# Optimization experiments

Hardware: AMD Instinct MI355X
Metric: run time of the kernel (lower is better)

The kernel has to match this reference:

```python
import jax, jax.numpy as jnp
import numpy as np
import math

FS = 256
NUM_SHOT = 5


def pe_table(L, d=FS):
    pos = np.arange(L, dtype=np.float32)[:, None]
    div = np.exp(np.arange(0, d, 2, dtype=np.float32) * (-math.log(10000.0) / float(d)))
    pe = np.zeros((L, d), dtype=np.float32)
    pe[:, 0::2] = np.sin(pos * div)
    pe[:, 1::2] = np.cos(pos * div)
    return jnp.asarray(pe)


def _conv(x, w, b, stride=1):
    pad = [(1, 1), (1, 1)] if w.shape[2] == 3 else [(0, 0), (0, 0)]
    y = jax.lax.conv_general_dilated(x, w, (stride, stride), pad,
                                     dimension_numbers=('NCHW', 'OIHW', 'NCHW'))
    return y + b[None, :, None, None]


def _up2(x):
    return jnp.repeat(jnp.repeat(x, 2, axis=2), 2, axis=3)


def setup_inputs() -> dict:
    key = jax.random.key(0)
    ks = iter(jax.random.split(key, 40))
    n = lambda shape, s=0.02: jax.random.normal(next(ks), shape, dtype=jnp.float32) * s
    inp = {
        'C3': jax.random.normal(next(ks), (8, 512, 40, 40), dtype=jnp.float32),
        'C4': jax.random.normal(next(ks), (8, 1024, 20, 20), dtype=jnp.float32),
        'C5': jax.random.normal(next(ks), (8, 2048, 10, 10), dtype=jnp.float32),
        'S3': jax.random.normal(next(ks), (40, 512, 40, 40), dtype=jnp.float32),
        'S4': jax.random.normal(next(ks), (40, 1024, 20, 20), dtype=jnp.float32),
        'S5': jax.random.normal(next(ks), (40, 2048, 10, 10), dtype=jnp.float32),
        'w_p3_1': n((FS, 512, 1, 1)), 'b_p3_1': jnp.zeros((FS,), jnp.float32),
        'w_p3_2': n((FS, FS, 3, 3)), 'b_p3_2': jnp.zeros((FS,), jnp.float32),
        'w_p4_1': n((FS, 1024, 1, 1)), 'b_p4_1': jnp.zeros((FS,), jnp.float32),
        'w_p4_2': n((FS, FS, 3, 3)), 'b_p4_2': jnp.zeros((FS,), jnp.float32),
        'w_p5_1': n((FS, 2048, 1, 1)), 'b_p5_1': jnp.zeros((FS,), jnp.float32),
        'w_p5_2': n((FS, FS, 3, 3)), 'b_p5_2': jnp.zeros((FS,), jnp.float32),
        'w_p6': n((FS, 2048, 3, 3)), 'b_p6': jnp.zeros((FS,), jnp.float32),
        'w_p7': n((FS, FS, 3, 3)), 'b_p7': jnp.zeros((FS,), jnp.float32),
        'wq': n((FS, FS), 0.01), 'bq': jnp.zeros((FS,), jnp.float32),
        'wk': n((FS, FS), 0.01), 'bk': jnp.zeros((FS,), jnp.float32),
    }
    return inp


def reference(C3, C4, C5, S3, S4, S5,
              w_p3_1, b_p3_1, w_p3_2, b_p3_2,
              w_p4_1, b_p4_1, w_p4_2, b_p4_2,
              w_p5_1, b_p5_1, w_p5_2, b_p5_2,
              w_p6, b_p6, w_p7, b_p7, wq, bq, wk, bk):
    B = C3.shape[0]
    # lateral 1x1 convs (shared between query and support)
    P5x = _conv(C5, w_p5_1, b_p5_1)
    P4x = _conv(C4, w_p4_1, b_p4_1)
    P3x = _conv(C3, w_p3_1, b_p3_1)
    P5s = _conv(S5, w_p5_1, b_p5_1)
    P4s = _conv(S4, w_p4_1, b_p4_1)
    P3s = _conv(S3, w_p3_1, b_p3_1)
    # P6/P7 heads
    P6x = _conv(C5, w_p6, b_p6, stride=2)
    P7x = _conv(jax.nn.relu(P6x), w_p7, b_p7, stride=2)
    P6s = _conv(S5, w_p6, b_p6, stride=2)
    P7s = _conv(jax.nn.relu(P6s), w_p7, b_p7, stride=2)
    # query-side top-down FPN
    P4x = _up2(P5x) + P4x
    P5x2 = _conv(P5x, w_p5_2, b_p5_2)
    P3x = P3x + _up2(P4x)
    P4x2 = _conv(P4x, w_p4_2, b_p4_2)
    P3x2 = _conv(P3x, w_p3_2, b_p3_2)
    # support: [B*S, C, h, w] -> [S, B, C, h, w]
    split = lambda x: x.reshape(B, NUM_SHOT, x.shape[1], x.shape[2], x.shape[3]).transpose(1, 0, 2, 3, 4)
    q_feats = [P3x2, P4x2, P5x2, P6x, P7x]
    s_feats = [split(P3s), split(P4s), split(P5s), split(P6s), split(P7s)]
    pes = [pe_table(h * w) for h, w in [(40, 40), (20, 20), (10, 10), (5, 5), (3, 3)]]
    scale = 1.0 / math.sqrt(float(FS))
    outs = []
    for qx, sx, pe in zip(q_feats, s_feats, pes):
        _, C, H, W = qx.shape
        q = qx.reshape(B, C, H * W).transpose(0, 2, 1)                       # [B, L, C]
        s = sx.reshape(NUM_SHOT, B, C, H * W).transpose(0, 1, 3, 2) + pe      # [S, B, L, C]
        Q = q @ wq.T + bq
        K = s @ wk.T + bk
        scores = jnp.einsum('blc,sbmc->sblm', Q, K) * scale                   # [S, B, L, L]
        A = jax.nn.softmax(scores, axis=-1)
        out = jnp.einsum('sblm,sbmc->blc', A, s) / NUM_SHOT                   # shot mean
        m = out.transpose(0, 2, 1).reshape(B, C, H, W)
        outs.append(jnp.concatenate([qx, m], axis=1))
    return tuple(outs)
```

## Files before the change

kernel.cpp:

```cpp
#include <hip/hip_runtime.h>

typedef unsigned short u16;
typedef __attribute__((ext_vector_type(8))) short short8;
typedef __attribute__((ext_vector_type(4))) float floatx4;

#define DEV static __device__ __forceinline__

DEV u16 f2bf(float f) {
    union { float f; unsigned u; } v; v.f = f;
    unsigned r = v.u + 0x7fff + ((v.u >> 16) & 1);
    return (u16)(r >> 16);
}
DEV float bf2f(u16 h) {
    union { unsigned u; float f; } v; v.u = ((unsigned)h) << 16;
    return v.f;
}

DEV void load_lds16(const u16* g, u16* l) {
    __builtin_amdgcn_global_load_lds(
        (const __attribute__((address_space(1))) void*)g,
        (__attribute__((address_space(3))) void*)l, 16, 0, 0);
}

#define FLAG_BF16 1
#define FLAG_AT   4
#define FLAG_PV   8

__global__ __launch_bounds__(256, 2) void gemm_nt(
    const u16* __restrict__ A, const u16* __restrict__ BT,
    const float* __restrict__ bias,
    u16* __restrict__ obf, float* __restrict__ oat, const float* __restrict__ lsum,
    int M, int K, int KS, int flags, int zoff,
    long sA, long sBT, long sBF, long sAT)
{
    __shared__ u16 Al[4096];
    __shared__ u16 Bl[4096];
    const int tid = threadIdx.x, lane = tid & 63, w = tid >> 6;
    const int wr = w & 1, wc = w >> 1;
    const int col16 = lane & 15, quad = (lane >> 4) & 3;
    const int mt = blockIdx.x, nt = blockIdx.y & 1, ks = blockIdx.y >> 1, z = blockIdx.z;
    const int sb = zoff + z;
    const int m0 = mt * 128, n0 = nt * 128;
    const u16* Ab = A + (size_t)z * sA;
    const u16* Bb = BT + (size_t)sb * sBT;
    const int Kper = K / KS;
    const int kbeg = ks * Kper;
    const floatx4 fz = {0.f, 0.f, 0.f, 0.f};

    floatx4 acc[4][4];
#pragma unroll
    for (int i = 0; i < 4; ++i)
#pragma unroll
        for (int j = 0; j < 4; ++j) acc[i][j] = fz;

    for (int kb = 0; kb < Kper; kb += 32) {
        const int k0 = kbeg + kb;
        __syncthreads();
#pragma unroll
        for (int i = 0; i < 2; ++i) {
            int cc = w * 2 + i;
            int q = cc >> 1;
            int row = (cc & 1) * 64 + lane;
            int rg = m0 + row; rg = rg < M ? rg : (M - 1);
            load_lds16(Ab + (size_t)rg * K + k0 + q * 8, &Al[cc * 512]);
            int nr = n0 + row;
            load_lds16(Bb + (size_t)nr * K + k0 + q * 8, &Bl[cc * 512]);
        }
        __syncthreads();
        short8 af[4], bfr[4];
#pragma unroll
        for (int i = 0; i < 4; ++i)
            af[i] = *(const short8*)&Al[(quad * 128 + wr * 64 + i * 16 + col16) * 8];
#pragma unroll
        for (int j = 0; j < 4; ++j)
            bfr[j] = *(const short8*)&Bl[(quad * 128 + wc * 64 + j * 16 + col16) * 8];
#pragma unroll
        for (int i = 0; i < 4; ++i)
#pragma unroll
            for (int j = 0; j < 4; ++j)
                acc[i][j] = __builtin_amdgcn_mfma_f32_16x16x32_bf16(af[i], bfr[j], acc[i][j], 0, 0, 0);
    }

#pragma unroll
    for (int j = 0; j < 4; ++j) {
        int gcol = n0 + wc * 64 + j * 16 + col16;
        float bv = (bias && ks == 0) ? bias[gcol] : 0.f;
#pragma unroll
        for (int i = 0; i < 4; ++i) {
            int rowb = m0 + wr * 64 + i * 16 + quad * 4;
#pragma unroll
            for (int r = 0; r < 4; ++r) {
                int row = rowb + r;
                if (row < M) {
                    float v = acc[i][j][r] + bv;
                    if (flags & FLAG_BF16) obf[(size_t)z * sBF + (size_t)row * 256 + gcol] = f2bf(v);
                    if (flags & FLAG_AT)   atomicAdd(&oat[(size_t)z * sAT + (size_t)row * 256 + gcol], v);
                    if (flags & FLAG_PV) {
                        int bl = z / 5;
                        float sc = 0.2f / lsum[(size_t)sb * 1664 + row];
                        atomicAdd(&oat[(size_t)bl * sAT + (size_t)row * 256 + gcol], v * sc);
                    }
                }
            }
        }
    }
}

__global__ __launch_bounds__(256, 2) void gemm_qk_exp(
    const u16* __restrict__ Q, const u16* __restrict__ Km,
    u16* __restrict__ eS, float* __restrict__ lsum,
    int M, int Kpad, int zoff)
{
    __shared__ u16 Al[4096];
    __shared__ u16 Bl[4096];
    const int tid = threadIdx.x, lane = tid & 63, w = tid >> 6;
    const int wr = w & 1, wc = w >> 1;
    const int col16 = lane & 15, quad = (lane >> 4) & 3;
    const int mt = blockIdx.x, nt = blockIdx.y, z = blockIdx.z;
    const int sb = zoff + z;
    const int m0 = mt * 128, n0 = nt * 128;
    const u16* Ab = Q + (size_t)(sb / 5) * M * 256;
    const u16* Bb = Km + (size_t)sb * M * 256;
    u16* eSb = eS + (size_t)z * M * Kpad;
    const floatx4 fz = {0.f, 0.f, 0.f, 0.f};

    floatx4 acc[4][4];
#pragma unroll
    for (int i = 0; i < 4; ++i)
#pragma unroll
        for (int j = 0; j < 4; ++j) acc[i][j] = fz;

    for (int k0 = 0; k0 < 256; k0 += 32) {
        __syncthreads();
#pragma unroll
        for (int i = 0; i < 2; ++i) {
            int cc = w * 2 + i;
            int q = cc >> 1;
            int row = (cc & 1) * 64 + lane;
            int rg = m0 + row; rg = rg < M ? rg : (M - 1);
            load_lds16(Ab + (size_t)rg * 256 + k0 + q * 8, &Al[cc * 512]);
            int nr = n0 + row; nr = nr < M ? nr : (M - 1);
            load_lds16(Bb + (size_t)nr * 256 + k0 + q * 8, &Bl[cc * 512]);
        }
        __syncthreads();
        short8 af[4], bfr[4];
#pragma unroll
        for (int i = 0; i < 4; ++i)
            af[i] = *(const short8*)&Al[(quad * 128 + wr * 64 + i * 16 + col16) * 8];
#pragma unroll
        for (int j = 0; j < 4; ++j)
            bfr[j] = *(const short8*)&Bl[(quad * 128 + wc * 64 + j * 16 + col16) * 8];
#pragma unroll
        for (int i = 0; i < 4; ++i)
#pragma unroll
            for (int j = 0; j < 4; ++j)
                acc[i][j] = __builtin_amdgcn_mfma_f32_16x16x32_bf16(af[i], bfr[j], acc[i][j], 0, 0, 0);
    }

#pragma unroll
    for (int i = 0; i < 4; ++i) {
#pragma unroll
        for (int r = 0; r < 4; ++r) {
            int row = m0 + wr * 64 + i * 16 + quad * 4 + r;
            float s = 0.f;
#pragma unroll
            for (int j = 0; j < 4; ++j) {
                int gcol = n0 + wc * 64 + j * 16 + col16;
                float v = 0.f;
                if (row < M && gcol < M) v = __expf(acc[i][j][r] * 0.0625f);
                u16 h = f2bf(v);
                if (row < M) eSb[(size_t)row * Kpad + gcol] = h;
                s += bf2f(h);
            }
            s += __shfl_xor(s, 1); s += __shfl_xor(s, 2);
            s += __shfl_xor(s, 4); s += __shfl_xor(s, 8);
            if ((lane & 15) == 0 && row < M)
                atomicAdd(&lsum[(size_t)sb * 1664 + row], s);
        }
    }
}


__global__ void transp_cast(const float* __restrict__ in, u16* __restrict__ out, int C, int HW) {
    __shared__ float t[32][33];
    int z = blockIdx.z;
    int p0 = blockIdx.x * 32, c0 = blockIdx.y * 32;
    int tx = threadIdx.x & 31, ty = threadIdx.x >> 5;
    const float* ib = in + (size_t)z * C * HW;
    u16* ob = out + (size_t)z * HW * C;
#pragma unroll
    for (int i = 0; i < 4; ++i) {
        int c = c0 + ty + i * 8, p = p0 + tx;
        t[ty + i * 8][tx] = (p < HW) ? ib[(size_t)c * HW + p] : 0.f;
    }
    __syncthreads();
#pragma unroll
    for (int i = 0; i < 4; ++i) {
        int p = p0 + ty + i * 8, c = c0 + tx;
        if (p < HW) ob[(size_t)p * C + c] = f2bf(t[tx][ty + i * 8]);
    }
}

__global__ void transp_bf(const u16* __restrict__ in, u16* __restrict__ out, int L, int Kpad) {
    __shared__ u16 t[32][33];
    int z = blockIdx.z;
    int l0 = blockIdx.x * 32, c0 = blockIdx.y * 32;
    int tx = threadIdx.x & 31, ty = threadIdx.x >> 5;
    const u16* ib = in + (size_t)z * L * 256;
    u16* ob = out + (size_t)z * 256 * Kpad;
#pragma unroll
    for (int i = 0; i < 4; ++i) {
        int l = l0 + ty + i * 8;
        t[ty + i * 8][tx] = (l < L) ? ib[(size_t)l * 256 + c0 + tx] : (u16)0;
    }
    __syncthreads();
#pragma unroll
    for (int i = 0; i < 4; ++i) {
        int l = l0 + tx, c = c0 + ty + i * 8;
        ob[(size_t)c * Kpad + l] = t[tx][ty + i * 8];
    }
}

__global__ void cast1d(const float* __restrict__ in, u16* __restrict__ out, long n) {
    long i = (long)blockIdx.x * 256 + threadIdx.x;
    if (i < n) out[i] = f2bf(in[i]);
}

__global__ void reorder_w3(const float* __restrict__ in, u16* __restrict__ out, int C) {
    long i = (long)blockIdx.x * 256 + threadIdx.x;
    int co = (int)(i / (9L * C));
    int r = (int)(i % (9L * C));
    int t = r / C, c = r % C;
    out[i] = f2bf(in[((size_t)co * C + c) * 9 + t]);
}

__global__ void im2col_s1(const u16* __restrict__ in, u16* __restrict__ out, int H, int Wd) {
    int z = blockIdx.y, p = blockIdx.x, c = threadIdx.x;
    int y = p / Wd, x = p % Wd;
    const u16* ib = in + (size_t)z * H * Wd * 256;
    u16* ob = out + ((size_t)z * H * Wd + p) * 2304;
#pragma unroll
    for (int t = 0; t < 9; ++t) {
        int ys = y + t / 3 - 1, xs = x + t % 3 - 1;
        u16 v = 0;
        if (ys >= 0 && ys < H && xs >= 0 && xs < Wd) v = ib[((size_t)ys * Wd + xs) * 256 + c];
        ob[t * 256 + c] = v;
    }
}

__global__ void im2col_s2(const u16* __restrict__ in, u16* __restrict__ out,
                          int Hin, int Win, int Hout, int Wout, int C, int relu) {
    int z = blockIdx.y, p = blockIdx.x, tid = threadIdx.x;
    int oy = p / Wout, ox = p % Wout;
    const u16* ib = in + (size_t)z * Hin * Win * C;
    u16* ob = out + ((size_t)z * Hout * Wout + p) * (9L * C);
    for (int t = 0; t < 9; ++t) {
        int ys = oy * 2 + t / 3 - 1, xs = ox * 2 + t % 3 - 1;
        bool ok = (ys >= 0 && ys < Hin && xs >= 0 && xs < Win);
        for (int c = tid; c < C; c += 256) {
            u16 v = 0;
            if (ok) {
                v = ib[((size_t)ys * Win + xs) * C + c];
                if (relu && (v & 0x8000)) v = 0;
            }
            ob[(size_t)t * C + c] = v;
        }
    }
}

__global__ void up2add(u16* __restrict__ big, const u16* __restrict__ small, int Hb, int Wb) {
    int z = blockIdx.y, p = blockIdx.x, c = threadIdx.x;
    int y = p / Wb, x = p % Wb;
    size_t bi = ((size_t)z * Hb * Wb + p) * 256 + c;
    size_t si = ((size_t)z * (Hb / 2) * (Wb / 2) + (size_t)(y >> 1) * (Wb / 2) + (x >> 1)) * 256 + c;
    big[bi] = f2bf(bf2f(big[bi]) + bf2f(small[si]));
}

__global__ void add_pe(u16* __restrict__ s, int L) {
    int z = blockIdx.y, l = blockIdx.x, c = threadIdx.x;
    size_t i = ((size_t)z * L + l) * 256 + c;
    float arg = (float)l * expf(-0.035977892078031971f * (float)(c & ~1));
    float pe = (c & 1) ? cosf(arg) : sinf(arg);
    s[i] = f2bf(bf2f(s[i]) + pe);
}

__global__ void cast_store(const float* __restrict__ in, u16* __restrict__ qout,
                           float* __restrict__ dout, int M, int choff) {
    __shared__ float t[32][33];
    int z = blockIdx.z, p0 = blockIdx.x * 32, c0 = blockIdx.y * 32;
    int tx = threadIdx.x & 31, ty = threadIdx.x >> 5;
#pragma unroll
    for (int i = 0; i < 4; ++i) {
        int p = p0 + ty + i * 8, c = c0 + tx;
        float v = 0.f;
        if (p < M) v = in[((size_t)z * M + p) * 256 + c];
        t[ty + i * 8][tx] = v;
        if (qout && p < M) qout[((size_t)z * M + p) * 256 + c] = f2bf(v);
    }
    __syncthreads();
    if (dout) {
#pragma unroll
        for (int i = 0; i < 4; ++i) {
            int p = p0 + tx, c = c0 + ty + i * 8;
            if (p < M) dout[((size_t)z * 512 + choff + c) * M + p] = t[tx][ty + i * 8];
        }
    }
}

extern "C" void kernel_launch(void* const* d_in, const int* in_sizes, int n_in,
                              void* d_out, int out_size, void* d_ws, size_t ws_size,
                              hipStream_t stream)
{
    (void)in_sizes; (void)n_in;
    const float* C3 = (const float*)d_in[0];
    const float* C4 = (const float*)d_in[1];
    const float* C5 = (const float*)d_in[2];
    const float* S3 = (const float*)d_in[3];
    const float* S4 = (const float*)d_in[4];
    const float* S5 = (const float*)d_in[5];
    const float* w31 = (const float*)d_in[6];  const float* b31 = (const float*)d_in[7];
    const float* w32 = (const float*)d_in[8];  const float* b32 = (const float*)d_in[9];
    const float* w41 = (const float*)d_in[10]; const float* b41 = (const float*)d_in[11];
    const float* w42 = (const float*)d_in[12]; const float* b42 = (const float*)d_in[13];
    const float* w51 = (const float*)d_in[14]; const float* b51 = (const float*)d_in[15];
    const float* w52 = (const float*)d_in[16]; const float* b52 = (const float*)d_in[17];
    const float* w6  = (const float*)d_in[18]; const float* b6  = (const float*)d_in[19];
    const float* w7  = (const float*)d_in[20]; const float* b7  = (const float*)d_in[21];
    const float* wq  = (const float*)d_in[22]; const float* bq  = (const float*)d_in[23];
    const float* wk  = (const float*)d_in[24]; const float* bk  = (const float*)d_in[25];
    float* out = (float*)d_out;

    char* base = (char*)d_ws;
    size_t off = 0;
    auto alloc = [&](size_t bytes) -> void* {
        void* r = base + off;
        off = (off + bytes + 255) & ~(size_t)255;
        return r;
    };

    char* arena = (char*)alloc(117964800);
    u16* X3t = (u16*)(arena + 0);
    u16* X4t = (u16*)(arena + 13107200);
    u16* S3t = (u16*)(arena + 19660800);
    u16* S4t = (u16*)(arena + 85196800);
    u16*   imcol   = (u16*)(arena + 0);
    float* convf32 = (float*)(arena + 58982400);
    u16*   expS    = (u16*)(arena + 0);
    float* attnf32 = (float*)(arena + 106496000);

    u16* X5t = (u16*)alloc((size_t)8  * 100 * 2048 * 2);
    u16* S5t = (u16*)alloc((size_t)40 * 100 * 2048 * 2);

    u16* w31b = (u16*)alloc(256L * 512 * 2);
    u16* w41b = (u16*)alloc(256L * 1024 * 2);
    u16* w51b = (u16*)alloc(256L * 2048 * 2);
    u16* wqb  = (u16*)alloc(256L * 256 * 2);
    u16* wkb  = (u16*)alloc(256L * 256 * 2);
    u16* w32b = (u16*)alloc(256L * 9 * 256 * 2);
    u16* w42b = (u16*)alloc(256L * 9 * 256 * 2);
    u16* w52b = (u16*)alloc(256L * 9 * 256 * 2);
    u16* w6b  = (u16*)alloc(256L * 9 * 2048 * 2);
    u16* w7b  = (u16*)alloc(256L * 9 * 256 * 2);

    u16* P3x = (u16*)alloc((size_t)8  * 1600 * 256 * 2);
    u16* P4x = (u16*)alloc((size_t)8  * 400  * 256 * 2);
    u16* P5x = (u16*)alloc((size_t)8  * 100  * 256 * 2);
    u16* P3s = (u16*)alloc((size_t)40 * 1600 * 256 * 2);
    u16* P4s = (u16*)alloc((size_t)40 * 400  * 256 * 2);
    u16* P5s = (u16*)alloc((size_t)40 * 100  * 256 * 2);
    u16* q3  = (u16*)alloc((size_t)8 * 1600 * 256 * 2);
    u16* q4  = (u16*)alloc((size_t)8 * 400  * 256 * 2);
    u16* q5  = (u16*)alloc((size_t)8 * 100  * 256 * 2);
    u16* q6  = (u16*)alloc((size_t)8 * 25   * 256 * 2);
    u16* q7  = (u16*)alloc((size_t)8 * 9    * 256 * 2);
    u16* P6sb = (u16*)alloc((size_t)40 * 25 * 256 * 2);
    u16* P7sb = (u16*)alloc((size_t)40 * 9  * 256 * 2);
    float* P6xf = (float*)alloc((size_t)8  * 25 * 256 * 4);
    float* P6sf = (float*)alloc((size_t)40 * 25 * 256 * 4);
    float* P7xf = (float*)alloc((size_t)8  * 9  * 256 * 4);
    float* P7sf = (float*)alloc((size_t)40 * 9  * 256 * 4);
    u16* Qb   = (u16*)alloc((size_t)8  * 1600 * 256 * 2);
    u16* Kb   = (u16*)alloc((size_t)40 * 1600 * 256 * 2);
    u16* sPeT = (u16*)alloc((size_t)40 * 256 * 1664 * 2);
    float* lsum = (float*)alloc((size_t)40 * 1664 * 4);

    if (off > ws_size) return;

    hipMemsetAsync(d_out, 0, (size_t)out_size * 4, stream);
    hipMemsetAsync(P6xf, 0, (size_t)8  * 25 * 256 * 4, stream);
    hipMemsetAsync(P6sf, 0, (size_t)40 * 25 * 256 * 4, stream);
    hipMemsetAsync(P7xf, 0, (size_t)8  * 9  * 256 * 4, stream);
    hipMemsetAsync(P7sf, 0, (size_t)40 * 9  * 256 * 4, stream);

    cast1d<<<dim3(512),  256, 0, stream>>>(w31, w31b, 256L * 512);
    cast1d<<<dim3(1024), 256, 0, stream>>>(w41, w41b, 256L * 1024);
    cast1d<<<dim3(2048), 256, 0, stream>>>(w51, w51b, 256L * 2048);
    cast1d<<<dim3(256),  256, 0, stream>>>(wq, wqb, 256L * 256);
    cast1d<<<dim3(256),  256, 0, stream>>>(wk, wkb, 256L * 256);
    reorder_w3<<<dim3(2304),  256, 0, stream>>>(w32, w32b, 256);
    reorder_w3<<<dim3(2304),  256, 0, stream>>>(w42, w42b, 256);
    reorder_w3<<<dim3(2304),  256, 0, stream>>>(w52, w52b, 256);
    reorder_w3<<<dim3(18432), 256, 0, stream>>>(w6, w6b, 2048);
    reorder_w3<<<dim3(2304),  256, 0, stream>>>(w7, w7b, 256);

    transp_cast<<<dim3(50, 16, 8),  256, 0, stream>>>(C3, X3t, 512, 1600);
    transp_cast<<<dim3(13, 32, 8),  256, 0, stream>>>(C4, X4t, 1024, 400);
    transp_cast<<<dim3(4,  64, 8),  256, 0, stream>>>(C5, X5t, 2048, 100);
    transp_cast<<<dim3(50, 16, 40), 256, 0, stream>>>(S3, S3t, 512, 1600);
    transp_cast<<<dim3(13, 32, 40), 256, 0, stream>>>(S4, S4t, 1024, 400);
    transp_cast<<<dim3(4,  64, 40), 256, 0, stream>>>(S5, S5t, 2048, 100);

    auto gemm = [&](const u16* A, const u16* BT, const float* bias,
                    u16* obf, float* oat, const float* ls,
                    int M, int K, int KS, int flags, int zoff,
                    long sA, long sBT, long sBF, long sAT, int nbz) {
        dim3 g((unsigned)((M + 127) / 128), (unsigned)(2 * KS), (unsigned)nbz);
        gemm_nt<<<g, 256, 0, stream>>>(A, BT, bias, obf, oat, ls, M, K, KS, flags, zoff,
                                       sA, sBT, sBF, sAT);
    };

    gemm(X3t, w31b, b31, P3x, 0, 0, 12800, 512,  1, FLAG_BF16, 0, 0, 0, 0, 0, 1);
    gemm(X4t, w41b, b41, P4x, 0, 0, 3200,  1024, 1, FLAG_BF16, 0, 0, 0, 0, 0, 1);
    gemm(X5t, w51b, b51, P5x, 0, 0, 800,   2048, 1, FLAG_BF16, 0, 0, 0, 0, 0, 1);
    gemm(S3t, w31b, b31, P3s, 0, 0, 64000, 512,  1, FLAG_BF16, 0, 0, 0, 0, 0, 1);
    gemm(S4t, w41b, b41, P4s, 0, 0, 16000, 1024, 1, FLAG_BF16, 0, 0, 0, 0, 0, 1);
    gemm(S5t, w51b, b51, P5s, 0, 0, 4000,  2048, 1, FLAG_BF16, 0, 0, 0, 0, 0, 1);

    const size_t lvl_off[5] = {0, 6553600, 8192000, 8601600, 8704000};

    im2col_s2<<<dim3(25, 8), 256, 0, stream>>>(X5t, imcol, 10, 10, 5, 5, 2048, 0);
    gemm(imcol, w6b, b6, 0, P6xf, 0, 200, 18432, 8, FLAG_AT, 0, 0, 0, 0, 0, 1);
    im2col_s2<<<dim3(25, 40), 256, 0, stream>>>(S5t, imcol, 10, 10, 5, 5, 2048, 0);
    gemm(imcol, w6b, b6, 0, P6sf, 0, 1000, 18432, 8, FLAG_AT, 0, 0, 0, 0, 0, 1);
    cast_store<<<dim3(1, 8, 8),  256, 0, stream>>>(P6xf, q6, out + lvl_off[3], 25, 0);
    cast_store<<<dim3(1, 8, 40), 256, 0, stream>>>(P6sf, P6sb, 0, 25, 0);
    im2col_s2<<<dim3(9, 8), 256, 0, stream>>>(q6, imcol, 5, 5, 3, 3, 256, 1);
    gemm(imcol, w7b, b7, 0, P7xf, 0, 72, 2304, 4, FLAG_AT, 0, 0, 0, 0, 0, 1);
    im2col_s2<<<dim3(9, 40), 256, 0, stream>>>(P6sb, imcol, 5, 5, 3, 3, 256, 1);
    gemm(imcol, w7b, b7, 0, P7sf, 0, 360, 2304, 4, FLAG_AT, 0, 0, 0, 0, 0, 1);
    cast_store<<<dim3(1, 8, 8),  256, 0, stream>>>(P7xf, q7, out + lvl_off[4], 9, 0);
    cast_store<<<dim3(1, 8, 40), 256, 0, stream>>>(P7sf, P7sb, 0, 9, 0);

    up2add<<<dim3(400, 8),  256, 0, stream>>>(P4x, P5x, 20, 20);
    up2add<<<dim3(1600, 8), 256, 0, stream>>>(P3x, P4x, 40, 40);

    im2col_s1<<<dim3(100, 8), 256, 0, stream>>>(P5x, imcol, 10, 10);
    hipMemsetAsync(convf32, 0, (size_t)8 * 100 * 256 * 4, stream);
    gemm(imcol, w52b, b52, 0, convf32, 0, 800, 2304, 4, FLAG_AT, 0, 0, 0, 0, 0, 1);
    cast_store<<<dim3(4, 8, 8), 256, 0, stream>>>(convf32, q5, out + lvl_off[2], 100, 0);

    im2col_s1<<<dim3(400, 8), 256, 0, stream>>>(P4x, imcol, 20, 20);
    hipMemsetAsync(convf32, 0, (size_t)8 * 400 * 256 * 4, stream);
    gemm(imcol, w42b, b42, 0, convf32, 0, 3200, 2304, 4, FLAG_AT, 0, 0, 0, 0, 0, 1);
    cast_store<<<dim3(13, 8, 8), 256, 0, stream>>>(convf32, q4, out + lvl_off[1], 400, 0);

    im2col_s1<<<dim3(1600, 8), 256, 0, stream>>>(P3x, imcol, 40, 40);
    hipMemsetAsync(convf32, 0, (size_t)8 * 1600 * 256 * 4, stream);
    gemm(imcol, w32b, b32, 0, convf32, 0, 12800, 2304, 4, FLAG_AT, 0, 0, 0, 0, 0, 1);
    cast_store<<<dim3(50, 8, 8), 256, 0, stream>>>(convf32, q3, out + lvl_off[0], 1600, 0);

    const int Ls[5]    = {1600, 400, 100, 25, 9};
    const int Kpads[5] = {1664, 512, 128, 128, 128};
    u16* qbuf[5] = {q3, q4, q5, q6, q7};
    u16* sbuf[5] = {P3s, P4s, P5s, P6sb, P7sb};
    for (int lv = 0; lv < 5; ++lv) {
        int L = Ls[lv], Kpad = Kpads[lv];
        add_pe<<<dim3(L, 40), 256, 0, stream>>>(sbuf[lv], L);
        transp_bf<<<dim3(Kpad / 32, 8, 40), 256, 0, stream>>>(sbuf[lv], sPeT, L, Kpad);
        gemm(qbuf[lv], wqb, bq, Qb, 0, 0, 8 * L,  256, 1, FLAG_BF16, 0, 0, 0, 0, 0, 1);
        gemm(sbuf[lv], wkb, bk, Kb, 0, 0, 40 * L, 256, 1, FLAG_BF16, 0, 0, 0, 0, 0, 1);
        hipMemsetAsync(lsum, 0, (size_t)40 * 1664 * 4, stream);
        int chunk = (lv == 0) ? 20 : 40;
        for (int c0 = 0; c0 < 40; c0 += chunk) {
            int nb = chunk / 5;
            hipMemsetAsync(attnf32, 0, (size_t)nb * L * 256 * 4, stream);
            dim3 gq((unsigned)((L + 127) / 128), (unsigned)(Kpad / 128), (unsigned)chunk);
            gemm_qk_exp<<<gq, 256, 0, stream>>>(Qb, Kb, expS, lsum, L, Kpad, c0);
            gemm(expS, sPeT, 0, 0, attnf32, lsum, L, Kpad, 1, FLAG_PV, c0,
                 (long)L * Kpad, (long)256 * Kpad, 0, (long)L * 256, chunk);
            cast_store<<<dim3((L + 31) / 32, 8, nb), 256, 0, stream>>>(
                attnf32, 0, out + lvl_off[lv] + (size_t)(c0 / 5) * 512 * L, L, 256);
        }
    }
}
```

Baseline: 2.321 ms.

## Double GEMM K-tile to 64 with XOR-swizzled LDS layout, retune split-K

Both the generic NT GEMM and the fused QK-exp GEMM now stage 64-wide K tiles per barrier instead of 32, doubling LDS buffers. Rows are stored contiguously in LDS with an XOR swizzle on 16-byte chunks so fragment reads avoid bank conflicts, and each tile runs two MFMA sub-steps. The aim is to halve barrier and load-issue overhead per unit of MFMA work. Split-K factors for two conv GEMMs are retuned to match; this needs K per split to divide by 64, and the larger LDS footprint may reduce occupancy.

```diff
diff --git a/kernel.cpp b/kernel.cpp
--- a/kernel.cpp
+++ b/kernel.cpp
@@ -33,11 +33,14 @@
     int M, int K, int KS, int flags, int zoff,
     long sA, long sBT, long sBF, long sAT)
 {
-    __shared__ u16 Al[4096];
-    __shared__ u16 Bl[4096];
+    __shared__ u16 Al[8192];
+    __shared__ u16 Bl[8192];
     const int tid = threadIdx.x, lane = tid & 63, w = tid >> 6;
     const int wr = w & 1, wc = w >> 1;
     const int col16 = lane & 15, quad = (lane >> 4) & 3;
+    const int lrow = lane >> 3;
+    const int lpc  = (lane & 7) ^ lrow;
+    const int sw   = col16 & 7;
     const int mt = blockIdx.x, nt = blockIdx.y & 1, ks = blockIdx.y >> 1, z = blockIdx.z;
     const int sb = zoff + z;
     const int m0 = mt * 128, n0 = nt * 128;
@@ -53,32 +56,38 @@
 #pragma unroll
         for (int j = 0; j < 4; ++j) acc[i][j] = fz;
 
-    for (int kb = 0; kb < Kper; kb += 32) {
+    for (int kb = 0; kb < Kper; kb += 64) {
         const int k0 = kbeg + kb;
         __syncthreads();
 #pragma unroll
-        for (int i = 0; i < 2; ++i) {
-            int cc = w * 2 + i;
-            int q = cc >> 1;
-            int row = (cc & 1) * 64 + lane;
-            int rg = m0 + row; rg = rg < M ? rg : (M - 1);
-            load_lds16(Ab + (size_t)rg * K + k0 + q * 8, &Al[cc * 512]);
-            int nr = n0 + row;
-            load_lds16(Bb + (size_t)nr * K + k0 + q * 8, &Bl[cc * 512]);
+        for (int j = 0; j < 4; ++j) {
+            int g = w * 4 + j;
+            int rloc = g * 8 + lrow;
+            int ra = m0 + rloc; ra = ra < M ? ra : (M - 1);
+            load_lds16(Ab + (size_t)ra * K + k0 + lpc * 8, &Al[g * 512]);
+            int rb = n0 + rloc;
+            load_lds16(Bb + (size_t)rb * K + k0 + lpc * 8, &Bl[g * 512]);
         }
         __syncthreads();
-        short8 af[4], bfr[4];
-#pragma unroll
-        for (int i = 0; i < 4; ++i)
-            af[i] = *(const short8*)&Al[(quad * 128 + wr * 64 + i * 16 + col16) * 8];
-#pragma unroll
-        for (int j = 0; j < 4; ++j)
-            bfr[j] = *(const short8*)&Bl[(quad * 128 + wc * 64 + j * 16 + col16) * 8];
-#pragma unroll
-        for (int i = 0; i < 4; ++i)
-#pragma unroll
-            for (int j = 0; j < 4; ++j)
-                acc[i][j] = __builtin_amdgcn_mfma_f32_16x16x32_bf16(af[i], bfr[j], acc[i][j], 0, 0, 0);
+#pragma unroll
+        for (int s = 0; s < 2; ++s) {
+            short8 af[4], bfr[4];
+#pragma unroll
+            for (int i = 0; i < 4; ++i) {
+                int r = wr * 64 + i * 16 + col16;
+                af[i] = *(const short8*)&Al[r * 64 + (((s * 4 + quad) ^ sw) * 8)];
+            }
+#pragma unroll
+            for (int j = 0; j < 4; ++j) {
+                int r = wc * 64 + j * 16 + col16;
+                bfr[j] = *(const short8*)&Bl[r * 64 + (((s * 4 + quad) ^ sw) * 8)];
+            }
+#pragma unroll
+            for (int i = 0; i < 4; ++i)
+#pragma unroll
+                for (int j = 0; j < 4; ++j)
+                    acc[i][j] = __builtin_amdgcn_mfma_f32_16x16x32_bf16(af[i], bfr[j], acc[i][j], 0, 0, 0);
+        }
     }
 
 #pragma unroll
@@ -111,11 +120,14 @@
     u16* __restrict__ eS, float* __restrict__ lsum,
     int M, int Kpad, int zoff)
 {
-    __shared__ u16 Al[4096];
-    __shared__ u16 Bl[4096];
+    __shared__ u16 Al[8192];
+    __shared__ u16 Bl[8192];
     const int tid = threadIdx.x, lane = tid & 63, w = tid >> 6;
     const int wr = w & 1, wc = w >> 1;
     const int col16 = lane & 15, quad = (lane >> 4) & 3;
+    const int lrow = lane >> 3;
+    const int lpc  = (lane & 7) ^ lrow;
+    const int sw   = col16 & 7;
     const int mt = blockIdx.x, nt = blockIdx.y, z = blockIdx.z;
     const int sb = zoff + z;
     const int m0 = mt * 128, n0 = nt * 128;
@@ -130,31 +142,37 @@
 #pragma unroll
         for (int j = 0; j < 4; ++j) acc[i][j] = fz;
 
-    for (int k0 = 0; k0 < 256; k0 += 32) {
+    for (int k0 = 0; k0 < 256; k0 += 64) {
         __syncthreads();
 #pragma unroll
-        for (int i = 0; i < 2; ++i) {
-            int cc = w * 2 + i;
-            int q = cc >> 1;
-            int row = (cc & 1) * 64 + lane;
-            int rg = m0 + row; rg = rg < M ? rg : (M - 1);
-            load_lds16(Ab + (size_t)rg * 256 + k0 + q * 8, &Al[cc * 512]);
-            int nr = n0 + row; nr = nr < M ? nr : (M - 1);
-            load_lds16(Bb + (size_t)nr * 256 + k0 + q * 8, &Bl[cc * 512]);
+        for (int j = 0; j < 4; ++j) {
+            int g = w * 4 + j;
+            int rloc = g * 8 + lrow;
+            int ra = m0 + rloc; ra = ra < M ? ra : (M - 1);
+            load_lds16(Ab + (size_t)ra * 256 + k0 + lpc * 8, &Al[g * 512]);
+            int rb = n0 + rloc; rb = rb < M ? rb : (M - 1);
+            load_lds16(Bb + (size_t)rb * 256 + k0 + lpc * 8, &Bl[g * 512]);
         }
         __syncthreads();
-        short8 af[4], bfr[4];
-#pragma unroll
-        for (int i = 0; i < 4; ++i)
-            af[i] = *(const short8*)&Al[(quad * 128 + wr * 64 + i * 16 + col16) * 8];
-#pragma unroll
-        for (int j = 0; j < 4; ++j)
-            bfr[j] = *(const short8*)&Bl[(quad * 128 + wc * 64 + j * 16 + col16) * 8];
-#pragma unroll
-        for (int i = 0; i < 4; ++i)
-#pragma unroll
-            for (int j = 0; j < 4; ++j)
-                acc[i][j] = __builtin_amdgcn_mfma_f32_16x16x32_bf16(af[i], bfr[j], acc[i][j], 0, 0, 0);
+#pragma unroll
+        for (int s = 0; s < 2; ++s) {
+            short8 af[4], bfr[4];
+#pragma unroll
+            for (int i = 0; i < 4; ++i) {
+                int r = wr * 64 + i * 16 + col16;
+                af[i] = *(const short8*)&Al[r * 64 + (((s * 4 + quad) ^ sw) * 8)];
+            }
+#pragma unroll
+            for (int j = 0; j < 4; ++j) {
+                int r = wc * 64 + j * 16 + col16;
+                bfr[j] = *(const short8*)&Bl[r * 64 + (((s * 4 + quad) ^ sw) * 8)];
+            }
+#pragma unroll
+            for (int i = 0; i < 4; ++i)
+#pragma unroll
+                for (int j = 0; j < 4; ++j)
+                    acc[i][j] = __builtin_amdgcn_mfma_f32_16x16x32_bf16(af[i], bfr[j], acc[i][j], 0, 0, 0);
+        }
     }
 
 #pragma unroll
@@ -446,7 +464,7 @@
 
     im2col_s1<<<dim3(100, 8), 256, 0, stream>>>(P5x, imcol, 10, 10);
     hipMemsetAsync(convf32, 0, (size_t)8 * 100 * 256 * 4, stream);
-    gemm(imcol, w52b, b52, 0, convf32, 0, 800, 2304, 4, FLAG_AT, 0, 0, 0, 0, 0, 1);
+    gemm(imcol, w52b, b52, 0, convf32, 0, 800, 2304, 6, FLAG_AT, 0, 0, 0, 0, 0, 1);
     cast_store<<<dim3(4, 8, 8), 256, 0, stream>>>(convf32, q5, out + lvl_off[2], 100, 0);
 
     im2col_s1<<<dim3(400, 8), 256, 0, stream>>>(P4x, imcol, 20, 20);
@@ -456,7 +474,7 @@
 
     im2col_s1<<<dim3(1600, 8), 256, 0, stream>>>(P3x, imcol, 40, 40);
     hipMemsetAsync(convf32, 0, (size_t)8 * 1600 * 256 * 4, stream);
-    gemm(imcol, w32b, b32, 0, convf32, 0, 12800, 2304, 4, FLAG_AT, 0, 0, 0, 0, 0, 1);
+    gemm(imcol, w32b, b32, 0, convf32, 0, 12800, 2304, 2, FLAG_AT, 0, 0, 0, 0, 0, 1);
     cast_store<<<dim3(50, 8, 8), 256, 0, stream>>>(convf32, q3, out + lvl_off[0], 1600, 0);
 
     const int Ls[5]    = {1600, 400, 100, 25, 9};
```

After: 1.943 ms. 1.19x faster.
